# Kernel optimization log

Hardware: AMD Instinct MI355X
Metric: run time of the kernel (lower is better)

## Reference

```python
import jax, jax.numpy as jnp
import numpy as np

P = 0.3            # swap probability (matches init_kwargs p)
H = 224
W = 224
PERM_SEED = 42     # fixed key so the reference is deterministic


def _index_permute(key, h, w, p):
    """Sequential random-neighbor swap permutation over an h*w grid.

    Faithful to CLOPLayer._index_permute: visit all flat indices in a random
    order; for each, with prob p swap it with one of its 4 toroidal neighbors
    (each with prob p/4). Implemented as a lax.scan over the visitation order
    (the swaps are inherently sequential / order-dependent).
    """
    n = h * w
    k1, k2 = jax.random.split(key)
    order = jax.random.permutation(k1, n)                       # visitation order
    probs = jnp.array([1.0 - p, p / 4, p / 4, p / 4, p / 4], dtype=jnp.float32)
    rs = jax.random.choice(k2, 5, shape=(n,), p=probs)          # move type per step

    def step(indexes, inp):
        idx, r = inp
        i = idx // w
        j = idx % w
        ip = jnp.where(r == 1, (i + 1) % h, jnp.where(r == 2, (i - 1) % h, i))
        jp = jnp.where(r == 3, (j + 1) % w, jnp.where(r == 4, (j - 1) % w, j))
        idx2 = jnp.where(r == 0, idx, ip * w + jp)              # r==0 -> self-swap (no-op)
        a = indexes[idx]
        b = indexes[idx2]
        indexes = indexes.at[idx].set(b).at[idx2].set(a)
        return indexes, None

    indexes = jnp.arange(n, dtype=jnp.int32)
    indexes, _ = jax.lax.scan(step, indexes, (order.astype(jnp.int32), rs.astype(jnp.int32)))
    return indexes


def setup_inputs() -> dict:
    key = jax.random.key(0)
    x = jax.random.normal(key, (128, 3, H, W), dtype=jnp.float32)
    return {"x": x}


def reference(x) -> jnp.ndarray:
    b, c, h, w = x.shape
    idx = _index_permute(jax.random.key(PERM_SEED), h, w, P)     # [h*w] int32
    flat = x.reshape(b, c, h * w)
    # torch.gather(flat, 2, idx broadcast over b,c) == take along last axis
    res = jnp.take(flat, idx, axis=2)
    return res.reshape(b, c, h, w)
```

## Files before the change

### kernel.cpp

```cpp
#include <hip/hip_runtime.h>
#include <cstdint>
#include <cstring>
#include <vector>
#include <algorithm>


#define PH 224
#define PW 224
#define PN (PH * PW)
#define NBC (128 * 3)

#define R_OUT 32
#define HALO 2
#define SR (R_OUT + 2 * HALO)
#define SRPW (SR * PW)
#define NWIN (PH / R_OUT)
#define KWIN (R_OUT * PW)
#define TPB 512
#define EMIT_IT (KWIN / (2 * TPB))
#define STAGE_F4 (SR * (PW / 4))
#define SITER ((STAGE_F4 + TPB - 1) / TPB)
#define OVF_CAP 1024

typedef float f4v __attribute__((ext_vector_type(4)));
typedef float f2v __attribute__((ext_vector_type(2)));

static inline uint32_t rotl32(uint32_t v, int d) {
  return (v << d) | (v >> (32 - d));
}

static void tf2x32(uint32_t k0, uint32_t k1, uint32_t x0, uint32_t x1,
                   uint32_t& o0, uint32_t& o1) {
  const uint32_t ks0 = k0, ks1 = k1, ks2 = k0 ^ k1 ^ 0x1BD11BDAu;
  uint32_t v0 = x0 + ks0;
  uint32_t v1 = x1 + ks1;
  static const int ra[4] = {13, 15, 26, 6};
  static const int rb[4] = {17, 29, 16, 24};
#define R4X(rr)                             \
  do {                                      \
    for (int _i = 0; _i < 4; ++_i) {        \
      v0 += v1;                             \
      v1 = rotl32(v1, (rr)[_i]);            \
      v1 ^= v0;                             \
    }                                       \
  } while (0)
  R4X(ra); v0 += ks1; v1 += ks2 + 1u;
  R4X(rb); v0 += ks2; v1 += ks0 + 2u;
  R4X(ra); v0 += ks0; v1 += ks1 + 3u;
  R4X(rb); v0 += ks1; v1 += ks2 + 4u;
  R4X(ra); v0 += ks2; v1 += ks0 + 5u;
#undef R4X
  o0 = v0;
  o1 = v1;
}

static void jax_split2(uint32_t k0, uint32_t k1,
                       uint32_t& a0, uint32_t& a1, uint32_t& b0, uint32_t& b1) {
  tf2x32(k0, k1, 0u, 0u, a0, a1);
  tf2x32(k0, k1, 0u, 1u, b0, b1);
}

static inline uint32_t jax_rb32(uint32_t k0, uint32_t k1, uint32_t i) {
  uint32_t y0, y1;
  tf2x32(k0, k1, 0u, i, y0, y1);
  return y0 ^ y1;
}

static std::vector<int> compute_perm() {
  const int n = PN;
  const uint32_t K0 = 0u, K1 = 42u;

  uint32_t k1a, k1b, k2a, k2b;
  jax_split2(K0, K1, k1a, k1b, k2a, k2b);

  std::vector<int> order(n);
  for (int i = 0; i < n; ++i) order[i] = i;
  uint32_t ck0 = k1a, ck1 = k1b;
  std::vector<std::pair<uint32_t, int>> kv(n);
  for (int round = 0; round < 2; ++round) {
    uint32_t nk0, nk1, sk0, sk1;
    jax_split2(ck0, ck1, nk0, nk1, sk0, sk1);
    ck0 = nk0; ck1 = nk1;
    for (int i = 0; i < n; ++i) {
      kv[i] = {jax_rb32(sk0, sk1, (uint32_t)i), order[i]};
    }
    std::stable_sort(kv.begin(), kv.end(),
                     [](const std::pair<uint32_t, int>& a,
                        const std::pair<uint32_t, int>& b) {
                       return a.first < b.first;
                     });
    for (int i = 0; i < n; ++i) order[i] = kv[i].second;
  }

  float probs[5] = {(float)(1.0 - 0.3), (float)(0.3 / 4), (float)(0.3 / 4),
                    (float)(0.3 / 4), (float)(0.3 / 4)};
  float pc[5];
  pc[0] = probs[0];
  for (int i = 1; i < 5; ++i) pc[i] = pc[i - 1] + probs[i];

  std::vector<uint8_t> rs(n);
  for (int i = 0; i < n; ++i) {
    uint32_t bits = jax_rb32(k2a, k2b, (uint32_t)i);
    uint32_t fb = (bits >> 9) | 0x3f800000u;
    float u;
    std::memcpy(&u, &fb, 4);
    u -= 1.0f;
    if (u < 0.0f) u = 0.0f;
    float r = pc[4] * (1.0f - u);
    int ind = (int)(std::lower_bound(pc, pc + 5, r) - pc);
    rs[i] = (uint8_t)ind;
  }

  std::vector<int> idx(n);
  for (int i = 0; i < n; ++i) idx[i] = i;
  for (int t = 0; t < n; ++t) {
    const int id = order[t];
    const int r = rs[t];
    const int i = id / PW, j = id % PW;
    int ip = i, jp = j;
    if (r == 1)      ip = (i + 1) % PH;
    else if (r == 2) ip = (i - 1 + PH) % PH;
    else if (r == 3) jp = (j + 1) % PW;
    else if (r == 4) jp = (j - 1 + PW) % PW;
    const int id2 = (r == 0) ? id : (ip * PW + jp);
    const int a = idx[id];
    const int b = idx[id2];
    idx[id]  = b;
    idx[id2] = a;
  }
  return idx;
}

static bool build_tables(const std::vector<int>& idx,
                         std::vector<uint16_t>& lofs, std::vector<int>& ovf,
                         std::vector<int>& cnt) {
  lofs.assign((size_t)NWIN * KWIN, 0);
  ovf.assign((size_t)NWIN * OVF_CAP, 0);
  cnt.assign(NWIN, 0);
  for (int w = 0; w < NWIN; ++w) {
    const int g0 = w * R_OUT - HALO;
    int no = 0;
    for (int kk = 0; kk < KWIN; ++kk) {
      const int k = w * KWIN + kk;
      const int s = idx[k];
      const int srow = s / PW, scol = s % PW;
      int i = ((srow - g0) % PH + PH) % PH;
      if (i < SR) {
        lofs[(size_t)w * KWIN + kk] = (uint16_t)(i * PW + scol);
      } else {
        if (no >= OVF_CAP) return false;
        ovf[(size_t)w * OVF_CAP + no] = s;
        lofs[(size_t)w * KWIN + kk] = (uint16_t)(SRPW + no);
        ++no;
      }
    }
    cnt[w] = no;
  }
  return true;
}

struct PermHolder {
  std::vector<int> h_idx;
  int* d_idx = nullptr;
  uint16_t* d_lofs = nullptr;
  int* d_ovf = nullptr;
  int* d_cnt = nullptr;
  bool lds_ok = false;

  PermHolder() {
    h_idx = compute_perm();

    int* p = nullptr;
    if (hipMalloc(&p, PN * sizeof(int)) == hipSuccess &&
        hipMemcpy(p, h_idx.data(), PN * sizeof(int),
                  hipMemcpyHostToDevice) == hipSuccess) {
      d_idx = p;
    }

    std::vector<uint16_t> lofs;
    std::vector<int> ovf, cnt;
    if (build_tables(h_idx, lofs, ovf, cnt)) {
      uint16_t* ql = nullptr;
      int* qo = nullptr;
      int* qc = nullptr;
      bool ok =
          hipMalloc(&ql, lofs.size() * sizeof(uint16_t)) == hipSuccess &&
          hipMemcpy(ql, lofs.data(), lofs.size() * sizeof(uint16_t),
                    hipMemcpyHostToDevice) == hipSuccess &&
          hipMalloc(&qo, ovf.size() * sizeof(int)) == hipSuccess &&
          hipMemcpy(qo, ovf.data(), ovf.size() * sizeof(int),
                    hipMemcpyHostToDevice) == hipSuccess &&
          hipMalloc(&qc, cnt.size() * sizeof(int)) == hipSuccess &&
          hipMemcpy(qc, cnt.data(), cnt.size() * sizeof(int),
                    hipMemcpyHostToDevice) == hipSuccess;
      if (ok) {
        d_lofs = ql;
        d_ovf = qo;
        d_cnt = qc;
        lds_ok = true;
      }
    }
  }
};
static PermHolder g_perm;

__global__ __launch_bounds__(TPB) void clop_glds(
    const float* __restrict__ x, const uint16_t* __restrict__ lofs,
    const int* __restrict__ ovf_idx, const int* __restrict__ ovf_cnt,
    float* __restrict__ out) {
  __shared__ float tile[SRPW + OVF_CAP];

  const int w = blockIdx.x;
  const size_t bc = blockIdx.y;
  const int g0 = w * R_OUT - HALO;
  const float* xs = x + bc * PN;

#pragma unroll
  for (int i = 0; i < SITER; ++i) {
    const int t = (int)threadIdx.x + i * TPB;
    if (t < STAGE_F4) {
      const int r = t / (PW / 4);
      const int j = (t % (PW / 4)) * 4;
      int g = g0 + r;
      if (g < 0) g += PH;
      else if (g >= PH) g -= PH;
      __builtin_amdgcn_global_load_lds(
          (const __attribute__((address_space(1))) void*)(xs + g * PW + j),
          (__attribute__((address_space(3))) void*)(tile + (size_t)t * 4),
          16, 0, 0);
    }
  }

  const uint32_t* lw2 = (const uint32_t*)(lofs + (size_t)w * KWIN);
  uint32_t o2[EMIT_IT];
#pragma unroll
  for (int i = 0; i < EMIT_IT; ++i)
    o2[i] = lw2[i * TPB + (int)threadIdx.x];

  const int novf = ovf_cnt[w];
  for (int t = (int)threadIdx.x; t < novf; t += TPB) {
    const int s = ovf_idx[w * OVF_CAP + t];
    __builtin_amdgcn_global_load_lds(
        (const __attribute__((address_space(1))) void*)(xs + s),
        (__attribute__((address_space(3))) void*)(tile + SRPW + t), 4, 0, 0);
  }

  __syncthreads();

  float* ob = out + bc * PN + (size_t)w * KWIN;
#pragma unroll
  for (int i = 0; i < EMIT_IT; ++i) {
    const uint32_t o = o2[i];
    f2v v;
    v.x = tile[o & 0xFFFFu];
    v.y = tile[o >> 16];
    __builtin_nontemporal_store(
        v, (f2v*)(ob + i * (2 * TPB) + 2 * (int)threadIdx.x));
  }
}

__global__ __launch_bounds__(256) void clop_gather4(
    const float* __restrict__ x, const int* __restrict__ idx,
    float* __restrict__ out) {
  const int w = blockIdx.x;
  const size_t bc = blockIdx.y;
  const int base = w * KWIN;
  const float* xs = x + bc * PN;
  float* ob = out + bc * PN + base;
  const int4* iv = (const int4*)(idx + base);

#pragma unroll
  for (int i = 0; i < 7; ++i) {
    const int g = i * 256 + (int)threadIdx.x;
    const int4 s = iv[g];
    f4v v;
    v.x = xs[s.x];
    v.y = xs[s.y];
    v.z = xs[s.z];
    v.w = xs[s.w];
    __builtin_nontemporal_store(v, (f4v*)(ob + (size_t)g * 4));
  }
}

extern "C" void kernel_launch(void* const* d_in, const int* in_sizes, int n_in,
                              void* d_out, int out_size, void* d_ws,
                              size_t ws_size, hipStream_t stream) {
  const float* x = (const float*)d_in[0];
  float* out = (float*)d_out;

  if (g_perm.lds_ok) {
    dim3 grid(NWIN, NBC);
    clop_glds<<<grid, TPB, 0, stream>>>(x, g_perm.d_lofs, g_perm.d_ovf,
                                        g_perm.d_cnt, out);
    return;
  }

  const int* idx;
  if (g_perm.d_idx != nullptr) {
    idx = g_perm.d_idx;
  } else {
    (void)hipMemcpyAsync(d_ws, g_perm.h_idx.data(), PN * sizeof(int),
                         hipMemcpyHostToDevice, stream);
    idx = (const int*)d_ws;
  }
  dim3 grid(NWIN, NBC);
  clop_gather4<<<grid, 256, 0, stream>>>(x, idx, out);
}
```

Measured before the change: 134.2 us.

## Shrink LDS gather window to 8 rows with templated halo selection

```diff
diff --git a/kernel.cpp b/kernel.cpp
--- a/kernel.cpp
+++ b/kernel.cpp
@@ -10,17 +10,12 @@
 #define PN (PH * PW)
 #define NBC (128 * 3)
 
-#define R_OUT 32
-#define HALO 2
-#define SR (R_OUT + 2 * HALO)
-#define SRPW (SR * PW)
+#define R_OUT 8
 #define NWIN (PH / R_OUT)
 #define KWIN (R_OUT * PW)
-#define TPB 512
+#define TPB 128
 #define EMIT_IT (KWIN / (2 * TPB))
-#define STAGE_F4 (SR * (PW / 4))
-#define SITER ((STAGE_F4 + TPB - 1) / TPB)
-#define OVF_CAP 1024
+#define OVF_CAP 192
 
 typedef float f4v __attribute__((ext_vector_type(4)));
 typedef float f2v __attribute__((ext_vector_type(2)));
@@ -131,26 +126,27 @@
   return idx;
 }
 
-static bool build_tables(const std::vector<int>& idx,
+static bool build_tables(const std::vector<int>& idx, int halo,
                          std::vector<uint16_t>& lofs, std::vector<int>& ovf,
                          std::vector<int>& cnt) {
+  const int sr = R_OUT + 2 * halo;
   lofs.assign((size_t)NWIN * KWIN, 0);
   ovf.assign((size_t)NWIN * OVF_CAP, 0);
   cnt.assign(NWIN, 0);
   for (int w = 0; w < NWIN; ++w) {
-    const int g0 = w * R_OUT - HALO;
+    const int g0 = w * R_OUT - halo;
     int no = 0;
     for (int kk = 0; kk < KWIN; ++kk) {
       const int k = w * KWIN + kk;
       const int s = idx[k];
       const int srow = s / PW, scol = s % PW;
       int i = ((srow - g0) % PH + PH) % PH;
-      if (i < SR) {
+      if (i < sr) {
         lofs[(size_t)w * KWIN + kk] = (uint16_t)(i * PW + scol);
       } else {
         if (no >= OVF_CAP) return false;
         ovf[(size_t)w * OVF_CAP + no] = s;
-        lofs[(size_t)w * KWIN + kk] = (uint16_t)(SRPW + no);
+        lofs[(size_t)w * KWIN + kk] = (uint16_t)(sr * PW + no);
         ++no;
       }
     }
@@ -165,7 +161,7 @@
   uint16_t* d_lofs = nullptr;
   int* d_ovf = nullptr;
   int* d_cnt = nullptr;
-  bool lds_ok = false;
+  int halo = 0;
 
   PermHolder() {
     h_idx = compute_perm();
@@ -177,9 +173,10 @@
       d_idx = p;
     }
 
-    std::vector<uint16_t> lofs;
-    std::vector<int> ovf, cnt;
-    if (build_tables(h_idx, lofs, ovf, cnt)) {
+    for (int h : {1, 2}) {
+      std::vector<uint16_t> lofs;
+      std::vector<int> ovf, cnt;
+      if (!build_tables(h_idx, h, lofs, ovf, cnt)) continue;
       uint16_t* ql = nullptr;
       int* qo = nullptr;
       int* qc = nullptr;
@@ -197,28 +194,33 @@
         d_lofs = ql;
         d_ovf = qo;
         d_cnt = qc;
-        lds_ok = true;
+        halo = h;
+        break;
       }
     }
   }
 };
 static PermHolder g_perm;
 
-__global__ __launch_bounds__(TPB) void clop_glds(
+template <int HALO_T>
+__global__ __launch_bounds__(TPB) void clop_small(
     const float* __restrict__ x, const uint16_t* __restrict__ lofs,
     const int* __restrict__ ovf_idx, const int* __restrict__ ovf_cnt,
     float* __restrict__ out) {
-  __shared__ float tile[SRPW + OVF_CAP];
+  constexpr int SR = R_OUT + 2 * HALO_T;
+  constexpr int STAGE = SR * (PW / 4);
+  constexpr int SITER = (STAGE + TPB - 1) / TPB;
+  __shared__ float tile[SR * PW + OVF_CAP];
 
   const int w = blockIdx.x;
   const size_t bc = blockIdx.y;
-  const int g0 = w * R_OUT - HALO;
+  const int g0 = w * R_OUT - HALO_T;
   const float* xs = x + bc * PN;
 
 #pragma unroll
   for (int i = 0; i < SITER; ++i) {
     const int t = (int)threadIdx.x + i * TPB;
-    if (t < STAGE_F4) {
+    if (t < STAGE) {
       const int r = t / (PW / 4);
       const int j = (t % (PW / 4)) * 4;
       int g = g0 + r;
@@ -242,7 +244,8 @@
     const int s = ovf_idx[w * OVF_CAP + t];
     __builtin_amdgcn_global_load_lds(
         (const __attribute__((address_space(1))) void*)(xs + s),
-        (__attribute__((address_space(3))) void*)(tile + SRPW + t), 4, 0, 0);
+        (__attribute__((address_space(3))) void*)(tile + SR * PW + t), 4, 0,
+        0);
   }
 
   __syncthreads();
@@ -264,7 +267,7 @@
     float* __restrict__ out) {
   const int w = blockIdx.x;
   const size_t bc = blockIdx.y;
-  const int base = w * KWIN;
+  const int base = w * (PN / 7);
   const float* xs = x + bc * PN;
   float* ob = out + bc * PN + base;
   const int4* iv = (const int4*)(idx + base);
@@ -288,10 +291,16 @@
   const float* x = (const float*)d_in[0];
   float* out = (float*)d_out;
 
-  if (g_perm.lds_ok) {
+  if (g_perm.halo == 1) {
     dim3 grid(NWIN, NBC);
-    clop_glds<<<grid, TPB, 0, stream>>>(x, g_perm.d_lofs, g_perm.d_ovf,
-                                        g_perm.d_cnt, out);
+    clop_small<1><<<grid, TPB, 0, stream>>>(x, g_perm.d_lofs, g_perm.d_ovf,
+                                            g_perm.d_cnt, out);
+    return;
+  }
+  if (g_perm.halo == 2) {
+    dim3 grid(NWIN, NBC);
+    clop_small<2><<<grid, TPB, 0, stream>>>(x, g_perm.d_lofs, g_perm.d_ovf,
+                                            g_perm.d_cnt, out);
     return;
   }
 
@@ -303,6 +312,6 @@
                          hipMemcpyHostToDevice, stream);
     idx = (const int*)d_ws;
   }
-  dim3 grid(NWIN, NBC);
+  dim3 grid(7, NBC);
   clop_gather4<<<grid, 256, 0, stream>>>(x, idx, out);
 }
```

Result: no change. 133.5 us (-0.5%).
